# Kernel optimization log

Hardware: AMD Instinct MI355X
Metric: run time of the kernel (lower is better)

The kernel has to match this reference:

```python
import jax, jax.numpy as jnp
import numpy as np
from jax import lax

B, L = 2, 5000            # images, candidate lines per image
C_IN, C_LOI = 256, 128    # backbone channels, dim_loi
H = W = 256               # feature-map spatial size (indices clamped to 255)
N_PTS0, N_PTS1 = 32, 8    # points sampled per line, after maxpool
POOL = N_PTS0 // N_PTS1   # MaxPool1d kernel/stride = 4
PLANES = C_LOI // 2       # Bottleneck1D mid channels
EPS = 1e-5


def setup_inputs() -> dict:
    key = jax.random.key(0)
    ks = jax.random.split(key, 16)
    f32 = jnp.float32
    s = 0.05
    feature = jax.random.normal(ks[0], (B, C_IN, H, W), f32)
    lines = jax.random.uniform(ks[1], (B, L, 2, 2), f32, minval=0.0, maxval=255.0)
    return {
        "feature": feature,
        "lines": lines,
        "fc1_w": jax.random.normal(ks[2], (C_LOI, C_IN), f32) * s,
        "fc1_b": jnp.zeros((C_LOI,), f32),
        "bn1_g": jnp.ones((C_LOI,), f32),
        "bn1_b": jnp.zeros((C_LOI,), f32),
        "bn1_m": jax.random.normal(ks[3], (C_LOI,), f32) * 0.1,
        "bn1_v": jax.random.uniform(ks[4], (C_LOI,), f32, minval=0.5, maxval=1.5),
        "conv1_w": jax.random.normal(ks[5], (PLANES, C_LOI), f32) * s,
        "conv1_b": jnp.zeros((PLANES,), f32),
        "bn2_g": jnp.ones((PLANES,), f32),
        "bn2_b": jnp.zeros((PLANES,), f32),
        "bn2_m": jax.random.normal(ks[6], (PLANES,), f32) * 0.1,
        "bn2_v": jax.random.uniform(ks[7], (PLANES,), f32, minval=0.5, maxval=1.5),
        "conv2_w": jax.random.normal(ks[8], (PLANES, PLANES, 3), f32) * s,
        "conv2_b": jnp.zeros((PLANES,), f32),
        "bn3_g": jnp.ones((PLANES,), f32),
        "bn3_b": jnp.zeros((PLANES,), f32),
        "bn3_m": jax.random.normal(ks[9], (PLANES,), f32) * 0.1,
        "bn3_v": jax.random.uniform(ks[10], (PLANES,), f32, minval=0.5, maxval=1.5),
        "conv3_w": jax.random.normal(ks[11], (C_LOI, PLANES), f32) * s,
        "conv3_b": jnp.zeros((C_LOI,), f32),
        "fc2_w": jax.random.normal(ks[12], (3, C_LOI * N_PTS1), f32) * s,
        "fc2_b": jnp.zeros((3,), f32),
    }


def _bn(x, g, b, m, v):
    # eval-mode BatchNorm1d over [N, C, T]
    inv = g / jnp.sqrt(v + EPS)
    return x * inv[None, :, None] + (b - m * inv)[None, :, None]


def _bilinear_sample(feat, lines):
    # feat: [B, C, H, W], lines: [B, L, 2, 2] -> [B, L, C, N_PTS0]
    lam = jnp.linspace(0.0, 1.0, N_PTS0, dtype=feat.dtype)[:, None]  # [P,1]
    # p = lam * endpoint0 + (1-lam) * endpoint1 - 0.5  -> [B, L, P, 2]
    p = lines[:, :, 0:1, :] * lam + lines[:, :, 1:2, :] * (1.0 - lam) - 0.5
    px, py = p[..., 0], p[..., 1]                       # [B, L, P]
    px0 = jnp.clip(jnp.floor(px), 0.0, 255.0)
    py0 = jnp.clip(jnp.floor(py), 0.0, 255.0)
    px1 = jnp.clip(px0 + 1.0, 0.0, 255.0)
    py1 = jnp.clip(py0 + 1.0, 0.0, 255.0)
    ix0, iy0 = px0.astype(jnp.int32), py0.astype(jnp.int32)
    ix1, iy1 = px1.astype(jnp.int32), py1.astype(jnp.int32)
    w00 = (px1 - px) * (py1 - py)
    w10 = (px - px0) * (py1 - py)
    w01 = (px1 - px) * (py - py0)
    w11 = (px - px0) * (py - py0)

    def one_image(f, a0, b0, a1, b1, c00, c10, c01, c11):
        # f: [C,H,W], indices/weights: [L,P] -> [C,L,P]
        return (f[:, a0, b0] * c00 + f[:, a1, b0] * c10 +
                f[:, a0, b1] * c01 + f[:, a1, b1] * c11)

    xp = jax.vmap(one_image)(feat, ix0, iy0, ix1, iy1, w00, w10, w01, w11)
    return jnp.transpose(xp, (0, 2, 1, 3))  # [B, L, C, P]


def _forward(feature, lines, fc1_w, fc1_b, bn1_g, bn1_b, bn1_m, bn1_v,
             conv1_w, conv1_b, bn2_g, bn2_b, bn2_m, bn2_v,
             conv2_w, conv2_b, bn3_g, bn3_b, bn3_m, bn3_v,
             conv3_w, conv3_b, fc2_w, fc2_b):
    # fc1: 1x1 conv over the backbone feature map
    x = jnp.einsum('oc,bchw->bohw', fc1_w, feature) + fc1_b[None, :, None, None]
    xp = _bilinear_sample(x, lines)                     # [B, L, C_LOI, P]
    xp = xp.reshape(B * L, C_LOI, N_PTS0)
    # MaxPool1d(kernel=POOL, stride=POOL)
    xp = xp.reshape(B * L, C_LOI, N_PTS1, POOL).max(axis=-1)  # [N, C, T]
    # Bottleneck1D residual branch: BN-ReLU-Conv1(k1)-BN-ReLU-Conv(k3)-BN-ReLU-Conv(k1)
    h = jax.nn.relu(_bn(xp, bn1_g, bn1_b, bn1_m, bn1_v))
    h = jnp.einsum('oc,nct->not', conv1_w, h) + conv1_b[None, :, None]
    h = jax.nn.relu(_bn(h, bn2_g, bn2_b, bn2_m, bn2_v))
    h = lax.conv_general_dilated(h, conv2_w, window_strides=(1,),
                                 padding=((1, 1),),
                                 dimension_numbers=('NCH', 'OIH', 'NCH'))
    h = h + conv2_b[None, :, None]
    h = jax.nn.relu(_bn(h, bn3_g, bn3_b, bn3_m, bn3_v))
    h = jnp.einsum('oc,nct->not', conv3_w, h) + conv3_b[None, :, None]
    xp = xp + h
    # fc2: ReLU + Linear(dim_loi * n_pts1 -> 3)
    flat = jax.nn.relu(xp).reshape(B * L, C_LOI * N_PTS1)
    return flat @ fc2_w.T + fc2_b


def reference(feature, lines, fc1_w, fc1_b, bn1_g, bn1_b, bn1_m, bn1_v,
              conv1_w, conv1_b, bn2_g, bn2_b, bn2_m, bn2_v,
              conv2_w, conv2_b, bn3_g, bn3_b, bn3_m, bn3_v,
              conv3_w, conv3_b, fc2_w, fc2_b):
    return _forward(feature, lines, fc1_w, fc1_b, bn1_g, bn1_b, bn1_m, bn1_v,
                    conv1_w, conv1_b, bn2_g, bn2_b, bn2_m, bn2_v,
                    conv2_w, conv2_b, bn3_g, bn3_b, bn3_m, bn3_v,
                    conv3_w, conv3_b, fc2_w, fc2_b)
```

## Files before the change

### kernel.cpp

```cpp
#include <hip/hip_runtime.h>
#include <hip/hip_bf16.h>

#define BB 2
#define LL 5000
#define CIN 256
#define CLOI 128
#define HH 256
#define WW 256
#define HWP (HH*WW)
#define NPTS0 32
#define NPTS1 8
#define PLANES 64
#define EPSV 1e-5f

#define X_BYTES   ((size_t)BB * HWP * CLOI * 2)
#define XS_BYTES  ((size_t)BB * LL * 1024 * 2)
#define W1S_OFF   (X_BYTES + XS_BYTES)
#define W2S_OFF   (W1S_OFF + 16384)
#define W3S_OFF   (W2S_OFF + 24576)
#define B1P_OFF   (W3S_OFF + 16384)
#define B2P_OFF   (B1P_OFF + 256)
#define S1_OFF    (B2P_OFF + 256)
#define T1_OFF    (S1_OFF + 512)
#define W0S_OFF   (T1_OFF + 512)

typedef unsigned int uint;
typedef unsigned short ushort;
typedef __attribute__((ext_vector_type(8))) short short8;
typedef __attribute__((ext_vector_type(4))) float f32x4;

__device__ __forceinline__ float bfLow(uint u)  { return __uint_as_float(u << 16); }
__device__ __forceinline__ float bfHigh(uint u) { return __uint_as_float(u & 0xffff0000u); }
__device__ __forceinline__ float bf2f(ushort u) { return __uint_as_float(((uint)u) << 16); }
__device__ __forceinline__ ushort f2bf(float f) {
    uint x = __float_as_uint(f);
    uint r = (x + 0x7fffu + ((x >> 16) & 1u)) >> 16;
    return (ushort)r;
}
__device__ __forceinline__ uint pk2(float a, float b) {
    float2 f; f.x = a; f.y = b;
    __hip_bfloat162 h = __float22bfloat162_rn(f);
    uint r;
    __builtin_memcpy(&r, &h, 4);
    return r;
}

__global__ __launch_bounds__(256) void fc1_kernel(
    const float* __restrict__ feature, const ushort* __restrict__ w0s,
    const float* __restrict__ fc1_b, ushort* __restrict__ xout)
{
    __shared__ ushort sF[32 * 64 * 8];

    int tid = threadIdx.x;
    int tile = blockIdx.x;
    int b = tile >> 10;
    int p0 = (tile & 1023) << 6;
    int wv = tid >> 6, lane = tid & 63;
    int q = lane >> 4, ln = lane & 15;

    short8 afr[8][2];
#pragma unroll
    for (int kg = 0; kg < 8; kg++)
#pragma unroll
        for (int mt = 0; mt < 2; mt++)
            afr[kg][mt] = *(const short8*)(w0s + ((size_t)((kg * 4 + q) * 128 + wv * 32 + mt * 16 + ln)) * 8);

    const float* fb = feature + (size_t)b * CIN * HWP + p0;
    int g_ = tid >> 4;
    int qd = tid & 15;
#pragma unroll
    for (int s = 0; s < 2; s++) {
        int g = s * 16 + g_;
        const float* src = fb + (size_t)(g * 8) * HWP + qd * 4;
        float4 rv[8];
#pragma unroll
        for (int j = 0; j < 8; j++) rv[j] = *(const float4*)(src + (size_t)j * HWP);
#pragma unroll
        for (int i = 0; i < 4; i++) {
            uint4 u;
            u.x = pk2(((const float*)&rv[0])[i], ((const float*)&rv[1])[i]);
            u.y = pk2(((const float*)&rv[2])[i], ((const float*)&rv[3])[i]);
            u.z = pk2(((const float*)&rv[4])[i], ((const float*)&rv[5])[i]);
            u.w = pk2(((const float*)&rv[6])[i], ((const float*)&rv[7])[i]);
            *(uint4*)(&sF[(g * 64 + qd * 4 + i) * 8]) = u;
        }
    }
    __syncthreads();

    const f32x4 fzero = { 0.f, 0.f, 0.f, 0.f };
    f32x4 acc[2][4];
#pragma unroll
    for (int mt = 0; mt < 2; mt++)
#pragma unroll
        for (int nt = 0; nt < 4; nt++) acc[mt][nt] = fzero;

#pragma unroll
    for (int kg = 0; kg < 8; kg++) {
#pragma unroll
        for (int nt = 0; nt < 4; nt++) {
            short8 bfr = *(short8*)(&sF[((kg * 4 + q) * 64 + nt * 16 + ln) * 8]);
            acc[0][nt] = __builtin_amdgcn_mfma_f32_16x16x32_bf16(afr[kg][0], bfr, acc[0][nt], 0, 0, 0);
            acc[1][nt] = __builtin_amdgcn_mfma_f32_16x16x32_bf16(afr[kg][1], bfr, acc[1][nt], 0, 0, 0);
        }
    }

    float bias[8];
    *(float4*)bias       = *(const float4*)(fc1_b + wv * 32 + q * 4);
    *(float4*)(bias + 4) = *(const float4*)(fc1_b + wv * 32 + 16 + q * 4);
    ushort* xrow = xout + (size_t)b * HWP * CLOI;
#pragma unroll
    for (int mt = 0; mt < 2; mt++)
#pragma unroll
        for (int nt = 0; nt < 4; nt++) {
            uint2 u;
            u.x = pk2(acc[mt][nt][0] + bias[mt * 4 + 0], acc[mt][nt][1] + bias[mt * 4 + 1]);
            u.y = pk2(acc[mt][nt][2] + bias[mt * 4 + 2], acc[mt][nt][3] + bias[mt * 4 + 3]);
            *(uint2*)(xrow + (size_t)(p0 + nt * 16 + ln) * CLOI + wv * 32 + mt * 16 + q * 4) = u;
        }
}

__global__ __launch_bounds__(256) void prep_kernel(
    const float* __restrict__ conv1_w, const float* __restrict__ conv1_b,
    const float* __restrict__ bn2_g, const float* __restrict__ bn2_b,
    const float* __restrict__ bn2_m, const float* __restrict__ bn2_v,
    const float* __restrict__ conv2_w, const float* __restrict__ conv2_b,
    const float* __restrict__ bn3_g, const float* __restrict__ bn3_b,
    const float* __restrict__ bn3_m, const float* __restrict__ bn3_v,
    const float* __restrict__ conv3_w,
    const float* __restrict__ bn1_g, const float* __restrict__ bn1_b,
    const float* __restrict__ bn1_m, const float* __restrict__ bn1_v,
    const float* __restrict__ fc1_w,
    ushort* __restrict__ w1s, ushort* __restrict__ w2s, ushort* __restrict__ w3s,
    float* __restrict__ b1p, float* __restrict__ b2p,
    float* __restrict__ s1o, float* __restrict__ t1o,
    ushort* __restrict__ w0s)
{
    int idx = blockIdx.x * 256 + threadIdx.x;
    if (idx < 8192) {
        int kg = idx >> 9, rem = idx & 511, m = rem >> 3, j = rem & 7;
        int c = kg * 8 + j;
        float s2 = bn2_g[m] * rsqrtf(bn2_v[m] + EPSV);
        w1s[idx] = f2bf(conv1_w[m * 128 + c] * s2);
    }
    if (idx < 12288) {
        int dt = idx >> 12, rem = idx & 4095;
        int kg = rem >> 9, m = (rem >> 3) & 63, j = rem & 7;
        int i = kg * 8 + j;
        float s3 = bn3_g[m] * rsqrtf(bn3_v[m] + EPSV);
        w2s[idx] = f2bf(conv2_w[m * 192 + i * 3 + dt] * s3);
    }
    if (idx < 8192) {
        int kg = idx >> 10, rem = idx & 1023, m = rem >> 3, j = rem & 7;
        w3s[idx] = f2bf(conv3_w[m * 64 + kg * 8 + j]);
    }
    if (idx < 32768) {
        int grp = idx >> 10, rem = idx & 1023, m = rem >> 3, j = rem & 7;
        w0s[idx] = f2bf(fc1_w[m * CIN + grp * 8 + j]);
    }
    if (idx < 64) {
        float s2 = bn2_g[idx] * rsqrtf(bn2_v[idx] + EPSV);
        b1p[idx] = conv1_b[idx] * s2 + bn2_b[idx] - bn2_m[idx] * s2;
        float s3 = bn3_g[idx] * rsqrtf(bn3_v[idx] + EPSV);
        b2p[idx] = conv2_b[idx] * s3 + bn3_b[idx] - bn3_m[idx] * s3;
    }
    if (idx < 128) {
        float s1 = bn1_g[idx] * rsqrtf(bn1_v[idx] + EPSV);
        s1o[idx] = s1;
        t1o[idx] = bn1_b[idx] - bn1_m[idx] * s1;
    }
}

__global__ __launch_bounds__(256) void sample_kernel(
    const ushort* __restrict__ x, const float* __restrict__ lines,
    ushort* __restrict__ xsb)
{
    __shared__ int    sBase[NPTS0];
    __shared__ float4 sW4[NPTS0];

    int n = blockIdx.x;
    int b = n / LL;
    int tid = threadIdx.x;

    if (tid < NPTS0) {
        int j = tid;
        float lam = (float)j * (1.0f / 31.0f);
        const float* lp = lines + (size_t)n * 4;
        float e0x = lp[0], e0y = lp[1], e1x = lp[2], e1y = lp[3];
        float px = e0x * lam + e1x * (1.f - lam) - 0.5f;
        float py = e0y * lam + e1y * (1.f - lam) - 0.5f;
        float px0 = fminf(fmaxf(floorf(px), 0.f), 255.f);
        float py0 = fminf(fmaxf(floorf(py), 0.f), 255.f);
        float px1 = px0 + 1.f;
        float py1 = py0 + 1.f;
        int ix0 = (int)px0, iy0 = (int)py0;
        sBase[j] = (ix0 * WW + iy0) * 256;
        float4 w;
        w.x = (px1 - px) * (py1 - py);
        w.y = (px - px0) * (py1 - py);
        w.z = (px1 - px) * (py - py0);
        w.w = (px - px0) * (py - py0);
        sW4[j] = w;
    }
    __syncthreads();

    int wv = tid >> 6, lane = tid & 63;
    bool hiHalf = lane >= 32;
    int loff = lane * 8;
    const char* xbc = (const char*)(x + (size_t)b * HWP * CLOI);

    float m0 = -INFINITY, m1 = -INFINITY, m2 = -INFINITY, m3 = -INFINITY;

#pragma unroll
    for (int jj = 0; jj < 8; jj++) {
        int j = wv * 8 + jj;
        int b0 = sBase[j];
        float4 w4 = sW4[j];
        int rb0 = __builtin_amdgcn_readfirstlane(b0);
        const char* pA = xbc + rb0;
        const char* pB = pA + 65536;
        uint2 l1 = *(const uint2*)(pA + loff);
        uint2 l2 = *(const uint2*)(pB + loff);
        float wA = hiHalf ? w4.z : w4.x;
        float wB = hiHalf ? w4.w : w4.y;
        float t0 = bfLow(l1.x) * wA + bfLow(l2.x) * wB;
        float t1 = bfHigh(l1.x) * wA + bfHigh(l2.x) * wB;
        float t2 = bfLow(l1.y) * wA + bfLow(l2.y) * wB;
        float t3 = bfHigh(l1.y) * wA + bfHigh(l2.y) * wB;
        t0 += __shfl_xor(t0, 32);
        t1 += __shfl_xor(t1, 32);
        t2 += __shfl_xor(t2, 32);
        t3 += __shfl_xor(t3, 32);
        if ((jj >= 4) == hiHalf) {
            m0 = fmaxf(m0, t0); m1 = fmaxf(m1, t1);
            m2 = fmaxf(m2, t2); m3 = fmaxf(m3, t3);
        }
    }

    int t = 2 * wv + (hiHalf ? 1 : 0);
    int c0 = (lane & 31) * 4;
    int kg = c0 >> 3;
    uint2 u; u.x = pk2(m0, m1); u.y = pk2(m2, m3);
    *(uint2*)(xsb + (size_t)n * 1024 + kg * 64 + t * 8 + (c0 & 7)) = u;
}

__global__ __launch_bounds__(256) void head_kernel(
    const ushort* __restrict__ xsb,
    const ushort* __restrict__ w1s, const ushort* __restrict__ w2s,
    const ushort* __restrict__ w3s,
    const float* __restrict__ b1p, const float* __restrict__ b2p,
    const float* __restrict__ s1g, const float* __restrict__ t1g,
    const float* __restrict__ conv3_b,
    const float* __restrict__ fc2_w, const float* __restrict__ fc2_b,
    float* __restrict__ out)
{
    __shared__ ushort sXS[8192];
    __shared__ ushort sH1[8192];
    __shared__ ushort sB2[4096];
    __shared__ float  sS1[128], sT1[128];
    __shared__ float  sB1[64], sB2b[64], sB3b[128];

    int tid = threadIdx.x;
    int wv = tid >> 6, lane = tid & 63;
    int q = lane >> 4, ln = lane & 15;
    int L0 = blockIdx.x * 8;
    int colg = wv * 16 + ln;

    if (tid < 128) { sS1[tid] = s1g[tid]; sT1[tid] = t1g[tid]; sB3b[tid] = conv3_b[tid]; }
    if (tid < 64)  { sB1[tid] = b1p[tid]; sB2b[tid] = b2p[tid]; }
    __syncthreads();

#pragma unroll
    for (int it = 0; it < 4; it++) {
        int ch = it * 256 + tid;
        int l = ch >> 7, wc = ch & 127;
        int kg = wc >> 3, tt = wc & 7;
        int col = l * 8 + tt;
        uint4 raw = *(const uint4*)(xsb + (size_t)(L0 + l) * 1024 + wc * 8);
        int off = (kg * 64 + col) * 8;
        *(uint4*)(&sXS[off]) = raw;
        uint rw[4] = { raw.x, raw.y, raw.z, raw.w };
        uint hw[4];
#pragma unroll
        for (int p = 0; p < 4; p++) {
            int c = kg * 8 + p * 2;
            float h0  = fmaxf(bfLow(rw[p])  * sS1[c]     + sT1[c],     0.f);
            float h1v = fmaxf(bfHigh(rw[p]) * sS1[c + 1] + sT1[c + 1], 0.f);
            hw[p] = pk2(h0, h1v);
        }
        uint4 hv; hv.x = hw[0]; hv.y = hw[1]; hv.z = hw[2]; hv.w = hw[3];
        *(uint4*)(&sH1[off]) = hv;
    }
    __syncthreads();

    const short8 bzero = { 0, 0, 0, 0, 0, 0, 0, 0 };
    const f32x4 fzero = { 0.f, 0.f, 0.f, 0.f };

    f32x4 acc1[4];
#pragma unroll
    for (int mt = 0; mt < 4; mt++) acc1[mt] = fzero;
#pragma unroll
    for (int ks = 0; ks < 4; ks++) {
        short8 b = *(short8*)(&sH1[((ks * 4 + q) * 64 + colg) * 8]);
#pragma unroll
        for (int mt = 0; mt < 4; mt++) {
            short8 a = *(const short8*)(w1s + ((ks * 4 + q) * 64 + mt * 16 + ln) * 8);
            acc1[mt] = __builtin_amdgcn_mfma_f32_16x16x32_bf16(a, b, acc1[mt], 0, 0, 0);
        }
    }
#pragma unroll
    for (int mt = 0; mt < 4; mt++) {
        int m0 = mt * 16 + q * 4;
        float v0 = fmaxf(acc1[mt][0] + sB1[m0 + 0], 0.f);
        float v1 = fmaxf(acc1[mt][1] + sB1[m0 + 1], 0.f);
        float v2 = fmaxf(acc1[mt][2] + sB1[m0 + 2], 0.f);
        float v3 = fmaxf(acc1[mt][3] + sB1[m0 + 3], 0.f);
        uint2 u; u.x = pk2(v0, v1); u.y = pk2(v2, v3);
        *(uint2*)(&sB2[((m0 >> 3) * 64 + colg) * 8 + (m0 & 7)]) = u;
    }
    __syncthreads();

    f32x4 acc2[4];
#pragma unroll
    for (int mt = 0; mt < 4; mt++) acc2[mt] = fzero;
    int tpos = colg & 7;
#pragma unroll
    for (int dt = 0; dt < 3; dt++) {
        int tsh = tpos + dt - 1;
        bool valid = ((unsigned)tsh < 8u);
        int colr = colg + dt - 1;
        colr = colr < 0 ? 0 : (colr > 63 ? 63 : colr);
#pragma unroll
        for (int ks = 0; ks < 2; ks++) {
            short8 b = *(short8*)(&sB2[((ks * 4 + q) * 64 + colr) * 8]);
            b = valid ? b : bzero;
#pragma unroll
            for (int mt = 0; mt < 4; mt++) {
                short8 a = *(const short8*)(w2s + dt * 4096 + ((ks * 4 + q) * 64 + mt * 16 + ln) * 8);
                acc2[mt] = __builtin_amdgcn_mfma_f32_16x16x32_bf16(a, b, acc2[mt], 0, 0, 0);
            }
        }
    }
#pragma unroll
    for (int mt = 0; mt < 4; mt++) {
        int m0 = mt * 16 + q * 4;
        float v0 = fmaxf(acc2[mt][0] + sB2b[m0 + 0], 0.f);
        float v1 = fmaxf(acc2[mt][1] + sB2b[m0 + 1], 0.f);
        float v2 = fmaxf(acc2[mt][2] + sB2b[m0 + 2], 0.f);
        float v3 = fmaxf(acc2[mt][3] + sB2b[m0 + 3], 0.f);
        uint2 u; u.x = pk2(v0, v1); u.y = pk2(v2, v3);
        *(uint2*)(&sH1[((m0 >> 3) * 64 + colg) * 8 + (m0 & 7)]) = u;
    }
    __syncthreads();

    f32x4 acc3[8];
#pragma unroll
    for (int mt = 0; mt < 8; mt++) acc3[mt] = fzero;
#pragma unroll
    for (int ks = 0; ks < 2; ks++) {
        short8 b = *(short8*)(&sH1[((ks * 4 + q) * 64 + colg) * 8]);
#pragma unroll
        for (int mt = 0; mt < 8; mt++) {
            short8 a = *(const short8*)(w3s + ((ks * 4 + q) * 128 + mt * 16 + ln) * 8);
            acc3[mt] = __builtin_amdgcn_mfma_f32_16x16x32_bf16(a, b, acc3[mt], 0, 0, 0);
        }
    }

    float p0 = 0.f, p1 = 0.f, p2 = 0.f;
#pragma unroll
    for (int mt = 0; mt < 8; mt++) {
        int m0 = mt * 16 + q * 4;
        int kg = m0 >> 3;
        uint2 xr = *(uint2*)(&sXS[kg * 512 + colg * 8 + (m0 & 7)]);
        float xsv[4] = { bfLow(xr.x), bfHigh(xr.x), bfLow(xr.y), bfHigh(xr.y) };
#pragma unroll
        for (int r = 0; r < 4; r++) {
            int m = m0 + r;
            float v = fmaxf(xsv[r] + acc3[mt][r] + sB3b[m], 0.f);
            int fi = m * 8 + tpos;
            p0 += v * fc2_w[fi];
            p1 += v * fc2_w[1024 + fi];
            p2 += v * fc2_w[2048 + fi];
        }
    }
    p0 += __shfl_xor(p0, 32); p1 += __shfl_xor(p1, 32); p2 += __shfl_xor(p2, 32);
    p0 += __shfl_xor(p0, 16); p1 += __shfl_xor(p1, 16); p2 += __shfl_xor(p2, 16);
    p0 += __shfl_xor(p0, 4);  p1 += __shfl_xor(p1, 4);  p2 += __shfl_xor(p2, 4);
    p0 += __shfl_xor(p0, 2);  p1 += __shfl_xor(p1, 2);  p2 += __shfl_xor(p2, 2);
    p0 += __shfl_xor(p0, 1);  p1 += __shfl_xor(p1, 1);  p2 += __shfl_xor(p2, 1);

    if (lane == 0 || lane == 8) {
        int line = L0 + wv * 2 + (lane >> 3);
        out[(size_t)line * 3 + 0] = p0 + fc2_b[0];
        out[(size_t)line * 3 + 1] = p1 + fc2_b[1];
        out[(size_t)line * 3 + 2] = p2 + fc2_b[2];
    }
}

extern "C" void kernel_launch(void* const* d_in, const int* in_sizes, int n_in,
                              void* d_out, int out_size, void* d_ws, size_t ws_size,
                              hipStream_t stream) {
    const float* feature = (const float*)d_in[0];
    const float* lines   = (const float*)d_in[1];
    const float* fc1_w   = (const float*)d_in[2];
    const float* fc1_b   = (const float*)d_in[3];
    const float* bn1_g   = (const float*)d_in[4];
    const float* bn1_b   = (const float*)d_in[5];
    const float* bn1_m   = (const float*)d_in[6];
    const float* bn1_v   = (const float*)d_in[7];
    const float* conv1_w = (const float*)d_in[8];
    const float* conv1_b = (const float*)d_in[9];
    const float* bn2_g   = (const float*)d_in[10];
    const float* bn2_b   = (const float*)d_in[11];
    const float* bn2_m   = (const float*)d_in[12];
    const float* bn2_v   = (const float*)d_in[13];
    const float* conv2_w = (const float*)d_in[14];
    const float* conv2_b = (const float*)d_in[15];
    const float* bn3_g   = (const float*)d_in[16];
    const float* bn3_b   = (const float*)d_in[17];
    const float* bn3_m   = (const float*)d_in[18];
    const float* bn3_v   = (const float*)d_in[19];
    const float* conv3_w = (const float*)d_in[20];
    const float* conv3_b = (const float*)d_in[21];
    const float* fc2_w   = (const float*)d_in[22];
    const float* fc2_b   = (const float*)d_in[23];
    float* out = (float*)d_out;

    char* ws = (char*)d_ws;
    ushort* x_bf = (ushort*)ws;
    ushort* xs_b = (ushort*)(ws + X_BYTES);
    ushort* w1s  = (ushort*)(ws + W1S_OFF);
    ushort* w2s  = (ushort*)(ws + W2S_OFF);
    ushort* w3s  = (ushort*)(ws + W3S_OFF);
    float*  b1p  = (float*)(ws + B1P_OFF);
    float*  b2p  = (float*)(ws + B2P_OFF);
    float*  s1g  = (float*)(ws + S1_OFF);
    float*  t1g  = (float*)(ws + T1_OFF);
    ushort* w0s  = (ushort*)(ws + W0S_OFF);

    prep_kernel<<<128, 256, 0, stream>>>(
        conv1_w, conv1_b, bn2_g, bn2_b, bn2_m, bn2_v,
        conv2_w, conv2_b, bn3_g, bn3_b, bn3_m, bn3_v,
        conv3_w, bn1_g, bn1_b, bn1_m, bn1_v, fc1_w,
        w1s, w2s, w3s, b1p, b2p, s1g, t1g, w0s);
    fc1_kernel<<<2048, 256, 0, stream>>>(feature, w0s, fc1_b, x_bf);
    sample_kernel<<<BB * LL, 256, 0, stream>>>(x_bf, lines, xs_b);
    head_kernel<<<BB * LL / 8, 256, 0, stream>>>(
        xs_b, w1s, w2s, w3s, b1p, b2p, s1g, t1g, conv3_b, fc2_w, fc2_b, out);
}
```

Baseline: 300.1 us.

## Fuse line sampling into head kernel and restructure fc2 reduction

Merges the per-line bilinear sampling and maxpool into the head kernel, so sampled features go straight to shared memory instead of round-tripping through a global workspace buffer. This also drops one kernel launch. The fc2 projection now stages the residual output in shared memory and uses vectorized weight loads with a full-wave reduction. fc1 loads its weight fragments per k-step instead of preloading them all, which lowers register pressure. The cost is fewer blocks doing the sampling work (8 lines per block, 1250 blocks), which may reduce the latency hiding available for the gathers.

```diff
diff --git a/kernel.cpp b/kernel.cpp
--- a/kernel.cpp
+++ b/kernel.cpp
@@ -14,8 +14,7 @@
 #define EPSV 1e-5f
 
 #define X_BYTES   ((size_t)BB * HWP * CLOI * 2)
-#define XS_BYTES  ((size_t)BB * LL * 1024 * 2)
-#define W1S_OFF   (X_BYTES + XS_BYTES)
+#define W1S_OFF   (X_BYTES)
 #define W2S_OFF   (W1S_OFF + 16384)
 #define W3S_OFF   (W2S_OFF + 24576)
 #define B1P_OFF   (W3S_OFF + 16384)
@@ -58,13 +57,6 @@
     int wv = tid >> 6, lane = tid & 63;
     int q = lane >> 4, ln = lane & 15;
 
-    short8 afr[8][2];
-#pragma unroll
-    for (int kg = 0; kg < 8; kg++)
-#pragma unroll
-        for (int mt = 0; mt < 2; mt++)
-            afr[kg][mt] = *(const short8*)(w0s + ((size_t)((kg * 4 + q) * 128 + wv * 32 + mt * 16 + ln)) * 8);
-
     const float* fb = feature + (size_t)b * CIN * HWP + p0;
     int g_ = tid >> 4;
     int qd = tid & 15;
@@ -96,11 +88,13 @@
 
 #pragma unroll
     for (int kg = 0; kg < 8; kg++) {
+        short8 a0 = *(const short8*)(w0s + ((size_t)((kg * 4 + q) * 128 + wv * 32 + ln)) * 8);
+        short8 a1 = *(const short8*)(w0s + ((size_t)((kg * 4 + q) * 128 + wv * 32 + 16 + ln)) * 8);
 #pragma unroll
         for (int nt = 0; nt < 4; nt++) {
             short8 bfr = *(short8*)(&sF[((kg * 4 + q) * 64 + nt * 16 + ln) * 8]);
-            acc[0][nt] = __builtin_amdgcn_mfma_f32_16x16x32_bf16(afr[kg][0], bfr, acc[0][nt], 0, 0, 0);
-            acc[1][nt] = __builtin_amdgcn_mfma_f32_16x16x32_bf16(afr[kg][1], bfr, acc[1][nt], 0, 0, 0);
+            acc[0][nt] = __builtin_amdgcn_mfma_f32_16x16x32_bf16(a0, bfr, acc[0][nt], 0, 0, 0);
+            acc[1][nt] = __builtin_amdgcn_mfma_f32_16x16x32_bf16(a1, bfr, acc[1][nt], 0, 0, 0);
         }
     }
 
@@ -170,21 +164,33 @@
     }
 }
 
-__global__ __launch_bounds__(256) void sample_kernel(
+__global__ __launch_bounds__(256) void fused_kernel(
     const ushort* __restrict__ x, const float* __restrict__ lines,
-    ushort* __restrict__ xsb)
+    const ushort* __restrict__ w1s, const ushort* __restrict__ w2s,
+    const ushort* __restrict__ w3s,
+    const float* __restrict__ b1p, const float* __restrict__ b2p,
+    const float* __restrict__ s1g, const float* __restrict__ t1g,
+    const float* __restrict__ conv3_b,
+    const float* __restrict__ fc2_w, const float* __restrict__ fc2_b,
+    float* __restrict__ out)
 {
-    __shared__ int    sBase[NPTS0];
-    __shared__ float4 sW4[NPTS0];
-
-    int n = blockIdx.x;
-    int b = n / LL;
+    __shared__ int    sGB[256];
+    __shared__ float4 sGW[256];
+    __shared__ ushort sXS[8192];
+    __shared__ ushort sH1[8192];
+    __shared__ ushort sB2[4096];
+    __shared__ float  sB1[64], sB2b[64], sB3b[128];
+
     int tid = threadIdx.x;
-
-    if (tid < NPTS0) {
-        int j = tid;
+    int wv = tid >> 6, lane = tid & 63;
+    int q = lane >> 4, ln = lane & 15;
+    int L0 = blockIdx.x * 8;
+    int colg = wv * 16 + ln;
+
+    {
+        int l = tid >> 5, j = tid & 31;
         float lam = (float)j * (1.0f / 31.0f);
-        const float* lp = lines + (size_t)n * 4;
+        const float* lp = lines + (size_t)(L0 + l) * 4;
         float e0x = lp[0], e0y = lp[1], e1x = lp[2], e1y = lp[3];
         float px = e0x * lam + e1x * (1.f - lam) - 0.5f;
         float py = e0y * lam + e1y * (1.f - lam) - 0.5f;
@@ -193,102 +199,67 @@
         float px1 = px0 + 1.f;
         float py1 = py0 + 1.f;
         int ix0 = (int)px0, iy0 = (int)py0;
-        sBase[j] = (ix0 * WW + iy0) * 256;
+        sGB[tid] = (ix0 * WW + iy0) * 256;
         float4 w;
         w.x = (px1 - px) * (py1 - py);
         w.y = (px - px0) * (py1 - py);
         w.z = (px1 - px) * (py - py0);
         w.w = (px - px0) * (py - py0);
-        sW4[j] = w;
-    }
+        sGW[tid] = w;
+    }
+    if (tid < 64)  { sB1[tid] = b1p[tid]; sB2b[tid] = b2p[tid]; }
+    if (tid < 128) sB3b[tid] = conv3_b[tid];
     __syncthreads();
 
-    int wv = tid >> 6, lane = tid & 63;
     bool hiHalf = lane >= 32;
     int loff = lane * 8;
+    int c0 = (lane & 31) * 4;
+    int kg0 = c0 >> 3, cr = c0 & 7;
+    float4 s1v = *(const float4*)(s1g + c0);
+    float4 t1v = *(const float4*)(t1g + c0);
+    int b = (L0 >= LL) ? 1 : 0;
     const char* xbc = (const char*)(x + (size_t)b * HWP * CLOI);
 
-    float m0 = -INFINITY, m1 = -INFINITY, m2 = -INFINITY, m3 = -INFINITY;
-
-#pragma unroll
-    for (int jj = 0; jj < 8; jj++) {
-        int j = wv * 8 + jj;
-        int b0 = sBase[j];
-        float4 w4 = sW4[j];
-        int rb0 = __builtin_amdgcn_readfirstlane(b0);
-        const char* pA = xbc + rb0;
-        const char* pB = pA + 65536;
-        uint2 l1 = *(const uint2*)(pA + loff);
-        uint2 l2 = *(const uint2*)(pB + loff);
-        float wA = hiHalf ? w4.z : w4.x;
-        float wB = hiHalf ? w4.w : w4.y;
-        float t0 = bfLow(l1.x) * wA + bfLow(l2.x) * wB;
-        float t1 = bfHigh(l1.x) * wA + bfHigh(l2.x) * wB;
-        float t2 = bfLow(l1.y) * wA + bfLow(l2.y) * wB;
-        float t3 = bfHigh(l1.y) * wA + bfHigh(l2.y) * wB;
-        t0 += __shfl_xor(t0, 32);
-        t1 += __shfl_xor(t1, 32);
-        t2 += __shfl_xor(t2, 32);
-        t3 += __shfl_xor(t3, 32);
-        if ((jj >= 4) == hiHalf) {
-            m0 = fmaxf(m0, t0); m1 = fmaxf(m1, t1);
-            m2 = fmaxf(m2, t2); m3 = fmaxf(m3, t3);
-        }
-    }
-
-    int t = 2 * wv + (hiHalf ? 1 : 0);
-    int c0 = (lane & 31) * 4;
-    int kg = c0 >> 3;
-    uint2 u; u.x = pk2(m0, m1); u.y = pk2(m2, m3);
-    *(uint2*)(xsb + (size_t)n * 1024 + kg * 64 + t * 8 + (c0 & 7)) = u;
-}
-
-__global__ __launch_bounds__(256) void head_kernel(
-    const ushort* __restrict__ xsb,
-    const ushort* __restrict__ w1s, const ushort* __restrict__ w2s,
-    const ushort* __restrict__ w3s,
-    const float* __restrict__ b1p, const float* __restrict__ b2p,
-    const float* __restrict__ s1g, const float* __restrict__ t1g,
-    const float* __restrict__ conv3_b,
-    const float* __restrict__ fc2_w, const float* __restrict__ fc2_b,
-    float* __restrict__ out)
-{
-    __shared__ ushort sXS[8192];
-    __shared__ ushort sH1[8192];
-    __shared__ ushort sB2[4096];
-    __shared__ float  sS1[128], sT1[128];
-    __shared__ float  sB1[64], sB2b[64], sB3b[128];
-
-    int tid = threadIdx.x;
-    int wv = tid >> 6, lane = tid & 63;
-    int q = lane >> 4, ln = lane & 15;
-    int L0 = blockIdx.x * 8;
-    int colg = wv * 16 + ln;
-
-    if (tid < 128) { sS1[tid] = s1g[tid]; sT1[tid] = t1g[tid]; sB3b[tid] = conv3_b[tid]; }
-    if (tid < 64)  { sB1[tid] = b1p[tid]; sB2b[tid] = b2p[tid]; }
-    __syncthreads();
-
-#pragma unroll
-    for (int it = 0; it < 4; it++) {
-        int ch = it * 256 + tid;
-        int l = ch >> 7, wc = ch & 127;
-        int kg = wc >> 3, tt = wc & 7;
-        int col = l * 8 + tt;
-        uint4 raw = *(const uint4*)(xsb + (size_t)(L0 + l) * 1024 + wc * 8);
-        int off = (kg * 64 + col) * 8;
-        *(uint4*)(&sXS[off]) = raw;
-        uint rw[4] = { raw.x, raw.y, raw.z, raw.w };
-        uint hw[4];
-#pragma unroll
-        for (int p = 0; p < 4; p++) {
-            int c = kg * 8 + p * 2;
-            float h0  = fmaxf(bfLow(rw[p])  * sS1[c]     + sT1[c],     0.f);
-            float h1v = fmaxf(bfHigh(rw[p]) * sS1[c + 1] + sT1[c + 1], 0.f);
-            hw[p] = pk2(h0, h1v);
-        }
-        uint4 hv; hv.x = hw[0]; hv.y = hw[1]; hv.z = hw[2]; hv.w = hw[3];
-        *(uint4*)(&sH1[off]) = hv;
+#pragma unroll
+    for (int li = 0; li < 2; li++) {
+        int l = wv * 2 + li;
+#pragma unroll
+        for (int c = 0; c < 4; c++) {
+            float m0 = -INFINITY, m1 = -INFINITY, m2 = -INFINITY, m3 = -INFINITY;
+#pragma unroll
+            for (int jj = 0; jj < 8; jj++) {
+                int gi = l * 32 + c * 8 + jj;
+                int rb0 = __builtin_amdgcn_readfirstlane(sGB[gi]);
+                float4 w4 = sGW[gi];
+                const char* pA = xbc + rb0;
+                uint2 l1 = *(const uint2*)(pA + loff);
+                uint2 l2 = *(const uint2*)(pA + 65536 + loff);
+                float wA = hiHalf ? w4.z : w4.x;
+                float wB = hiHalf ? w4.w : w4.y;
+                float t0 = bfLow(l1.x) * wA + bfLow(l2.x) * wB;
+                float t1 = bfHigh(l1.x) * wA + bfHigh(l2.x) * wB;
+                float t2 = bfLow(l1.y) * wA + bfLow(l2.y) * wB;
+                float t3 = bfHigh(l1.y) * wA + bfHigh(l2.y) * wB;
+                t0 += __shfl_xor(t0, 32);
+                t1 += __shfl_xor(t1, 32);
+                t2 += __shfl_xor(t2, 32);
+                t3 += __shfl_xor(t3, 32);
+                if ((jj >= 4) == hiHalf) {
+                    m0 = fmaxf(m0, t0); m1 = fmaxf(m1, t1);
+                    m2 = fmaxf(m2, t2); m3 = fmaxf(m3, t3);
+                }
+            }
+            int t = 2 * c + (hiHalf ? 1 : 0);
+            int off = (kg0 * 64 + l * 8 + t) * 8 + cr;
+            uint2 u; u.x = pk2(m0, m1); u.y = pk2(m2, m3);
+            *(uint2*)(&sXS[off]) = u;
+            float h0 = fmaxf(m0 * s1v.x + t1v.x, 0.f);
+            float h1 = fmaxf(m1 * s1v.y + t1v.y, 0.f);
+            float h2 = fmaxf(m2 * s1v.z + t1v.z, 0.f);
+            float h3 = fmaxf(m3 * s1v.w + t1v.w, 0.f);
+            uint2 hu; hu.x = pk2(h0, h1); hu.y = pk2(h2, h3);
+            *(uint2*)(&sH1[off]) = hu;
+        }
     }
     __syncthreads();
 
@@ -300,11 +271,11 @@
     for (int mt = 0; mt < 4; mt++) acc1[mt] = fzero;
 #pragma unroll
     for (int ks = 0; ks < 4; ks++) {
-        short8 b = *(short8*)(&sH1[((ks * 4 + q) * 64 + colg) * 8]);
+        short8 bfr = *(short8*)(&sH1[((ks * 4 + q) * 64 + colg) * 8]);
 #pragma unroll
         for (int mt = 0; mt < 4; mt++) {
             short8 a = *(const short8*)(w1s + ((ks * 4 + q) * 64 + mt * 16 + ln) * 8);
-            acc1[mt] = __builtin_amdgcn_mfma_f32_16x16x32_bf16(a, b, acc1[mt], 0, 0, 0);
+            acc1[mt] = __builtin_amdgcn_mfma_f32_16x16x32_bf16(a, bfr, acc1[mt], 0, 0, 0);
         }
     }
 #pragma unroll
@@ -331,12 +302,12 @@
         colr = colr < 0 ? 0 : (colr > 63 ? 63 : colr);
 #pragma unroll
         for (int ks = 0; ks < 2; ks++) {
-            short8 b = *(short8*)(&sB2[((ks * 4 + q) * 64 + colr) * 8]);
-            b = valid ? b : bzero;
+            short8 bfr = *(short8*)(&sB2[((ks * 4 + q) * 64 + colr) * 8]);
+            bfr = valid ? bfr : bzero;
 #pragma unroll
             for (int mt = 0; mt < 4; mt++) {
                 short8 a = *(const short8*)(w2s + dt * 4096 + ((ks * 4 + q) * 64 + mt * 16 + ln) * 8);
-                acc2[mt] = __builtin_amdgcn_mfma_f32_16x16x32_bf16(a, b, acc2[mt], 0, 0, 0);
+                acc2[mt] = __builtin_amdgcn_mfma_f32_16x16x32_bf16(a, bfr, acc2[mt], 0, 0, 0);
             }
         }
     }
@@ -357,42 +328,65 @@
     for (int mt = 0; mt < 8; mt++) acc3[mt] = fzero;
 #pragma unroll
     for (int ks = 0; ks < 2; ks++) {
-        short8 b = *(short8*)(&sH1[((ks * 4 + q) * 64 + colg) * 8]);
+        short8 bfr = *(short8*)(&sH1[((ks * 4 + q) * 64 + colg) * 8]);
 #pragma unroll
         for (int mt = 0; mt < 8; mt++) {
             short8 a = *(const short8*)(w3s + ((ks * 4 + q) * 128 + mt * 16 + ln) * 8);
-            acc3[mt] = __builtin_amdgcn_mfma_f32_16x16x32_bf16(a, b, acc3[mt], 0, 0, 0);
-        }
-    }
-
-    float p0 = 0.f, p1 = 0.f, p2 = 0.f;
+            acc3[mt] = __builtin_amdgcn_mfma_f32_16x16x32_bf16(a, bfr, acc3[mt], 0, 0, 0);
+        }
+    }
+
 #pragma unroll
     for (int mt = 0; mt < 8; mt++) {
         int m0 = mt * 16 + q * 4;
         int kg = m0 >> 3;
-        uint2 xr = *(uint2*)(&sXS[kg * 512 + colg * 8 + (m0 & 7)]);
-        float xsv[4] = { bfLow(xr.x), bfHigh(xr.x), bfLow(xr.y), bfHigh(xr.y) };
-#pragma unroll
-        for (int r = 0; r < 4; r++) {
-            int m = m0 + r;
-            float v = fmaxf(xsv[r] + acc3[mt][r] + sB3b[m], 0.f);
-            int fi = m * 8 + tpos;
-            p0 += v * fc2_w[fi];
-            p1 += v * fc2_w[1024 + fi];
-            p2 += v * fc2_w[2048 + fi];
-        }
-    }
-    p0 += __shfl_xor(p0, 32); p1 += __shfl_xor(p1, 32); p2 += __shfl_xor(p2, 32);
-    p0 += __shfl_xor(p0, 16); p1 += __shfl_xor(p1, 16); p2 += __shfl_xor(p2, 16);
-    p0 += __shfl_xor(p0, 4);  p1 += __shfl_xor(p1, 4);  p2 += __shfl_xor(p2, 4);
-    p0 += __shfl_xor(p0, 2);  p1 += __shfl_xor(p1, 2);  p2 += __shfl_xor(p2, 2);
-    p0 += __shfl_xor(p0, 1);  p1 += __shfl_xor(p1, 1);  p2 += __shfl_xor(p2, 1);
-
-    if (lane == 0 || lane == 8) {
-        int line = L0 + wv * 2 + (lane >> 3);
-        out[(size_t)line * 3 + 0] = p0 + fc2_b[0];
-        out[(size_t)line * 3 + 1] = p1 + fc2_b[1];
-        out[(size_t)line * 3 + 2] = p2 + fc2_b[2];
+        uint2 xr = *(uint2*)(&sXS[(kg * 64 + colg) * 8 + (m0 & 7)]);
+        float v0 = fmaxf(bfLow(xr.x)  + acc3[mt][0] + sB3b[m0 + 0], 0.f);
+        float v1 = fmaxf(bfHigh(xr.x) + acc3[mt][1] + sB3b[m0 + 1], 0.f);
+        float v2 = fmaxf(bfLow(xr.y)  + acc3[mt][2] + sB3b[m0 + 2], 0.f);
+        float v3 = fmaxf(bfHigh(xr.y) + acc3[mt][3] + sB3b[m0 + 3], 0.f);
+        uint2 u; u.x = pk2(v0, v1); u.y = pk2(v2, v3);
+        *(uint2*)(&sH1[(kg * 64 + colg) * 8 + (m0 & 7)]) = u;
+    }
+
+    {
+        const float4* fw4 = (const float4*)fc2_w;
+        int la = wv * 2;
+        float pa0 = 0.f, pa1 = 0.f, pa2 = 0.f;
+        float pb0 = 0.f, pb1 = 0.f, pb2 = 0.f;
+#pragma unroll
+        for (int it = 0; it < 4; it++) {
+            int idx4 = it * 64 + lane;
+            int cc = idx4 >> 1;
+            int th = (idx4 & 1) * 4;
+            float4 w0 = fw4[idx4];
+            float4 w1 = fw4[256 + idx4];
+            float4 w2 = fw4[512 + idx4];
+            int basea = ((cc >> 3) * 64 + la * 8 + th) * 8 + (cc & 7);
+            float va[4], vb[4];
+#pragma unroll
+            for (int i = 0; i < 4; i++) {
+                va[i] = bf2f(sH1[basea + i * 8]);
+                vb[i] = bf2f(sH1[basea + 64 + i * 8]);
+            }
+            pa0 += va[0] * w0.x + va[1] * w0.y + va[2] * w0.z + va[3] * w0.w;
+            pa1 += va[0] * w1.x + va[1] * w1.y + va[2] * w1.z + va[3] * w1.w;
+            pa2 += va[0] * w2.x + va[1] * w2.y + va[2] * w2.z + va[3] * w2.w;
+            pb0 += vb[0] * w0.x + vb[1] * w0.y + vb[2] * w0.z + vb[3] * w0.w;
+            pb1 += vb[0] * w1.x + vb[1] * w1.y + vb[2] * w1.z + vb[3] * w1.w;
+            pb2 += vb[0] * w2.x + vb[1] * w2.y + vb[2] * w2.z + vb[3] * w2.w;
+        }
+#pragma unroll
+        for (int off = 32; off > 0; off >>= 1) {
+            pa0 += __shfl_xor(pa0, off); pa1 += __shfl_xor(pa1, off); pa2 += __shfl_xor(pa2, off);
+            pb0 += __shfl_xor(pb0, off); pb1 += __shfl_xor(pb1, off); pb2 += __shfl_xor(pb2, off);
+        }
+        if (lane == 0) {
+            float f0 = fc2_b[0], f1 = fc2_b[1], f2 = fc2_b[2];
+            size_t oa = (size_t)(L0 + la) * 3;
+            out[oa + 0] = pa0 + f0; out[oa + 1] = pa1 + f1; out[oa + 2] = pa2 + f2;
+            out[oa + 3] = pb0 + f0; out[oa + 4] = pb1 + f1; out[oa + 5] = pb2 + f2;
+        }
     }
 }
 
@@ -427,7 +421,6 @@
 
     char* ws = (char*)d_ws;
     ushort* x_bf = (ushort*)ws;
-    ushort* xs_b = (ushort*)(ws + X_BYTES);
     ushort* w1s  = (ushort*)(ws + W1S_OFF);
     ushort* w2s  = (ushort*)(ws + W2S_OFF);
     ushort* w3s  = (ushort*)(ws + W3S_OFF);
@@ -443,7 +436,6 @@
         conv3_w, bn1_g, bn1_b, bn1_m, bn1_v, fc1_w,
         w1s, w2s, w3s, b1p, b2p, s1g, t1g, w0s);
     fc1_kernel<<<2048, 256, 0, stream>>>(feature, w0s, fc1_b, x_bf);
-    sample_kernel<<<BB * LL, 256, 0, stream>>>(x_bf, lines, xs_b);
-    head_kernel<<<BB * LL / 8, 256, 0, stream>>>(
-        xs_b, w1s, w2s, w3s, b1p, b2p, s1g, t1g, conv3_b, fc2_w, fc2_b, out);
-}
+    fused_kernel<<<BB * LL / 8, 256, 0, stream>>>(
+        x_bf, lines, w1s, w2s, w3s, b1p, b2p, s1g, t1g, conv3_b, fc2_w, fc2_b, out);
+}
```

Result: slower. 324.4 us (+8.1%).
